# Performance work log

Hardware: AMD Instinct MI355X
Metric: run time of the kernel (lower is better)

The kernel has to match this reference:

```python
import jax, jax.numpy as jnp
import numpy as np

DT = 0.1  # integration step
EPS = 1e-06

def setup_inputs() -> dict:
    key = jax.random.key(0)
    ks = jax.random.split(key, 8)
    B, T, I, H, O = 256, 512, 64, 512, 64
    return {
        'x_seq': jax.random.normal(ks[0], (B, T, I), jnp.float32),
        'W_in0': jax.random.normal(ks[1], (H, I), jnp.float32) * (1.0 / np.sqrt(I)),
        'b_in0': jnp.zeros((H,), jnp.float32),
        'A0':    jax.random.normal(ks[2], (H, H), jnp.float32) * 0.1,
        'tau0':  jnp.ones((H,), jnp.float32),
        'W_in1': jax.random.normal(ks[3], (H, H), jnp.float32) * (1.0 / np.sqrt(H)),
        'b_in1': jnp.zeros((H,), jnp.float32),
        'A1':    jax.random.normal(ks[4], (H, H), jnp.float32) * 0.1,
        'tau1':  jnp.ones((H,), jnp.float32),
        'W_out': jax.random.normal(ks[5], (O, H), jnp.float32) * (1.0 / np.sqrt(H)),
        'b_out': jnp.zeros((O,), jnp.float32),
    }

def _euler(h, drive, A, tau):
    # dh/dt = (1/|tau|+eps) * (-h + tanh(h @ A.T + drive)); Euler step
    inv_tau = 1.0 / (jnp.abs(tau) + EPS)
    dh = inv_tau * (-h + jnp.tanh(h @ A.T + drive))
    return h + DT * dh

def reference(x_seq, W_in0, b_in0, A0, tau0, W_in1, b_in1, A1, tau1, W_out, b_out):
    B, T, _ = x_seq.shape
    H = A0.shape[0]
    # layer-0 input projection is time-independent of hidden state: precompute
    xw = jnp.einsum('bti,hi->bth', x_seq, W_in0) + b_in0  # (B, T, H)

    def step(carry, xw_t):
        h0, h1 = carry
        h0 = _euler(h0, xw_t, A0, tau0)
        h1 = _euler(h1, h0 @ W_in1.T + b_in1, A1, tau1)
        y = h1 @ W_out.T + b_out
        return (h0, h1), y

    h0 = jnp.zeros((B, H), x_seq.dtype)
    h1 = jnp.zeros((B, H), x_seq.dtype)
    _, ys = jax.lax.scan(step, (h0, h1), jnp.swapaxes(xw, 0, 1))  # scan over time
    return jnp.swapaxes(ys, 0, 1)  # (B, T, O)
```

## Files before the change

kernel.cpp:

```cpp
#include <hip/hip_runtime.h>
#include <hip/hip_bf16.h>
#include <stdint.h>

#define B_ 256
#define T_ 512
#define I_ 64
#define H_ 512
#define O_ 64
#define DT_ 0.1f
#define EPS_ 1e-6f
#define SCALE_ 2048.0f
#define INVSCALE_ 4.8828125e-4f

typedef _Float16 f16x8 __attribute__((ext_vector_type(8)));
typedef float    f32x4 __attribute__((ext_vector_type(4)));

__device__ __forceinline__ f32x4 mfma16(f16x8 a, f16x8 b, f32x4 c) {
    return __builtin_amdgcn_mfma_f32_16x16x32_f16(a, b, c, 0, 0, 0);
}
__device__ __forceinline__ float fast_tanh(float x) {
    float e = __expf(2.0f * x);
    return 1.0f - 2.0f / (e + 1.0f);
}
__device__ __forceinline__ bool is_f32_input(const void* tau0) {
    return *(const unsigned int*)tau0 == 0x3F800000u;
}
__device__ __forceinline__ float load_any(const void* p, int i, bool f32) {
    return f32 ? ((const float*)p)[i] : (float)((const __bf16*)p)[i];
}
__device__ __forceinline__ _Float16 f16bits(unsigned short u) {
    union { unsigned short u; _Float16 f; } c; c.u = u; return c.f;
}
__device__ __forceinline__ unsigned short bits16(_Float16 f) {
    union { unsigned short u; _Float16 f; } c; c.f = f; return c.u;
}
__device__ __forceinline__ int bsum8(uint32_t v) {
    return (int)((v & 0xFF) + ((v >> 8) & 0xFF) + ((v >> 16) & 0xFF) + ((v >> 24) & 0xFF));
}
__device__ __forceinline__ int bmax8(uint32_t v) {
    int a = (int)(v & 0xFF), b = (int)((v >> 8) & 0xFF);
    int c = (int)((v >> 16) & 0xFF), d = (int)((v >> 24) & 0xFF);
    int x = a > b ? a : b, y = c > d ? c : d;
    return x > y ? x : y;
}

#define WS_A0H 0u
#define WS_A1H 524288u
#define WS_W1H 1048576u
#define WS_A0L 1572864u
#define WS_A1L 2097152u
#define WS_W1L 2621440u
#define WS_W0H 3145728u
#define WS_W0L 3211264u
#define WS_WOP 3276800u
#define WS_IT0 3407872u
#define WS_IT1 3409920u
#define WS_BI0 3411968u
#define WS_BI1 3414016u
#define WS_BO  3416064u
#define WS_FLGP 3538944u
#define WS_XCD2 3604480u
#define WS_HB0  4194304u
#define WS_HB1  6291456u

__global__ void k_swizzle(const void* __restrict__ src, _Float16* __restrict__ hi,
                          _Float16* __restrict__ lo, int NK, int kshift,
                          const void* __restrict__ tau) {
    bool f32 = is_f32_input(tau);
    int i = blockIdx.x * 256 + threadIdx.x;
    if (i >= NK) return;
    int n = i >> kshift;
    int k = i & ((1 << kshift) - 1);
    float v = load_any(src, i, f32);
    _Float16 h = (_Float16)v;
    _Float16 l = (_Float16)((v - (float)h) * SCALE_);
    int tile = n >> 4, m = n & 15, kk = k >> 5, q = (k >> 3) & 3, j = k & 7;
    int Kst = 1 << (kshift - 5);
    int off = ((tile * Kst + kk) << 9) + (((q << 4) | m) << 3) + j;
    hi[off] = h;
    lo[off] = l;
}

__global__ void k_swzwo(const void* __restrict__ src, _Float16* __restrict__ dst,
                        const void* __restrict__ tau) {
    bool f32 = is_f32_input(tau);
    int i = blockIdx.x * 256 + threadIdx.x;
    if (i >= 65536) return;
    int j = i & 7, l = (i >> 3) & 63, kk = (i >> 9) & 15, cg = i >> 13;
    int m = l & 15, q = l >> 4;
    int k = kk * 32 + q * 8 + j;
    float v = (m < 8) ? load_any(src, (8 * cg + m) * H_ + k, f32) : 0.0f;
    dst[i] = (_Float16)v;
}

__global__ void k_params(const void* t0, const void* t1,
                         const void* b0, const void* b1, const void* bo,
                         float* it0, float* it1, float* b0f, float* b1f, float* bof) {
    bool f32 = is_f32_input(t0);
    int i = threadIdx.x;
    if (i < H_) {
        it0[i] = 1.0f / (fabsf(load_any(t0, i, f32)) + EPS_);
        it1[i] = 1.0f / (fabsf(load_any(t1, i, f32)) + EPS_);
        b0f[i] = load_any(b0, i, f32);
        b1f[i] = load_any(b1, i, f32);
    }
    if (i < O_) bof[i] = load_any(bo, i, f32);
}

__global__ void k_zero(uint32_t* p, int n) {
    int i = blockIdx.x * 256 + threadIdx.x;
    if (i < n) p[i] = 0;
}

__device__ __forceinline__ void waitflag(const uint32_t* p, uint32_t tgt) {
    while (__hip_atomic_load(p, __ATOMIC_RELAXED, __HIP_MEMORY_SCOPE_AGENT) < tgt) { }
    __asm__ __volatile__("" ::: "memory");
}

__global__ __launch_bounds__(256, 1) void liquid_kernel(
    const void* __restrict__ x_seq, const void* __restrict__ tau0probe,
    char* __restrict__ ws, void* __restrict__ out)
{
    __shared__ _Float16 hTh[2][16][520], hTl[2][16][520];
    __shared__ float yscr[4][16][16];
    __shared__ int s_fast;

    const bool f32 = is_f32_input(tau0probe);
    const int tid  = threadIdx.x;
    const int lane = tid & 63;
    const int w    = tid >> 6;
    const int m    = lane & 15;
    const int q    = lane >> 4;
    const int koff = q * 8;
    const int rg   = blockIdx.x;
    const int cg   = blockIdx.y;
    const int chain = blockIdx.z;
    const int r0   = rg * 16;
    const int colg = cg * 64 + w * 16 + m;
    const int tlg  = cg * 4 + w;
    const int c0   = w * 128 + lane;
    const int c1   = c0 + 64;

    uint32_t* ring = (uint32_t*)(ws + WS_HB0);
    uint32_t* hb1  = (uint32_t*)(ws + WS_HB1);
    uint32_t* fpad = (uint32_t*)(ws + WS_FLGP);
    uint32_t* fsf  = fpad +         (size_t)rg * 8 * 32;
    uint32_t* f1f  = fpad + 4096  + (size_t)rg * 8 * 32;
    uint32_t* pg1  = fpad + 12288 + (size_t)rg * 8 * 32;

    {
        uint32_t* xc = (uint32_t*)(ws + WS_XCD2) + (size_t)rg * 32;
        if (tid == 0) {
            int xid = (int)(__builtin_amdgcn_s_getreg((3u << 11) | 20u) & 7u);
            __hip_atomic_fetch_add(xc + (xid >> 2), 1u << (8 * (xid & 3)),
                                   __ATOMIC_RELAXED, __HIP_MEMORY_SCOPE_AGENT);
            uint32_t v0, v1;
            do {
                __builtin_amdgcn_s_sleep(1);
                v0 = __hip_atomic_load(xc,     __ATOMIC_RELAXED, __HIP_MEMORY_SCOPE_AGENT);
                v1 = __hip_atomic_load(xc + 1, __ATOMIC_RELAXED, __HIP_MEMORY_SCOPE_AGENT);
            } while (bsum8(v0) + bsum8(v1) < 16);
            int mx0 = bmax8(v0), mx1 = bmax8(v1);
            s_fast = ((mx0 > mx1 ? mx0 : mx1) == 16) ? 1 : 0;
        }
    }

    const float* bow = (const float*)(ws + WS_BO);
    const float boY  = (m < 8) ? bow[cg * 8 + m] : 0.0f;

    __syncthreads();
    const bool fastp = (s_fast != 0);

    if (chain == 0) {
        const float it0c = ((const float*)(ws + WS_IT0))[colg];
        const float bi0c = ((const float*)(ws + WS_BI0))[colg];
        const size_t fb  = (((size_t)(tlg * 16)) << 9) + (lane << 3);
        const size_t fb0 = (((size_t)(tlg * 2))  << 9) + (lane << 3);
        f16x8 cA0h[16], cA0l[16];
#pragma unroll
        for (int kk = 0; kk < 16; ++kk) {
            cA0h[kk] = *(const f16x8*)((const _Float16*)(ws + WS_A0H) + fb + ((size_t)kk << 9));
            cA0l[kk] = *(const f16x8*)((const _Float16*)(ws + WS_A0L) + fb + ((size_t)kk << 9));
        }
        f16x8 cW0h[2], cW0l[2];
#pragma unroll
        for (int kk = 0; kk < 2; ++kk) {
            cW0h[kk] = *(const f16x8*)((const _Float16*)(ws + WS_W0H) + fb0 + ((size_t)kk << 9));
            cW0l[kk] = *(const f16x8*)((const _Float16*)(ws + WS_W0L) + fb0 + ((size_t)kk << 9));
        }
        const float*  xpf = (const float*) x_seq + (size_t)(r0 + m) * T_ * I_ + koff;
        const __bf16* xpb = (const __bf16*)x_seq + (size_t)(r0 + m) * T_ * I_ + koff;
        float h0m[4] = {0.f, 0.f, 0.f, 0.f};

        f32x4 xf0 = {}, xf1 = {}, xf2 = {}, xf3 = {};
        uint4 xb0 = {}, xb1 = {};
        if (f32) {
            xf0 = *(const f32x4*)(xpf);
            xf1 = *(const f32x4*)(xpf + 4);
            xf2 = *(const f32x4*)(xpf + 32);
            xf3 = *(const f32x4*)(xpf + 36);
        } else {
            xb0 = *(const uint4*)(xpb);
            xb1 = *(const uint4*)(xpb + 32);
        }

        for (int s = 0; s < T_; ++s) {
            const int cur = s & 1;
            const int rs4 = s & 3;
            const int ws4 = (s + 1) & 3;

            waitflag(fsf + (size_t)(2 * w) * 32,     4u * (uint32_t)s);
            waitflag(fsf + (size_t)(2 * w + 1) * 32, 4u * (uint32_t)s);
            uint32_t rv0[16], rv1[16];
            {
                const uint32_t* src = ring + ((size_t)(rs4 * 16 + rg) * 16) * 512;
                if (fastp) {
#pragma unroll
                    for (int k = 0; k < 16; ++k) {
                        rv0[k] = src[(size_t)k * 512 + c0];
                        rv1[k] = src[(size_t)k * 512 + c1];
                    }
                } else {
#pragma unroll
                    for (int k = 0; k < 16; ++k) {
                        rv0[k] = __hip_atomic_load(src + (size_t)k * 512 + c0, __ATOMIC_RELAXED, __HIP_MEMORY_SCOPE_AGENT);
                        rv1[k] = __hip_atomic_load(src + (size_t)k * 512 + c1, __ATOMIC_RELAXED, __HIP_MEMORY_SCOPE_AGENT);
                    }
                }
            }
#pragma unroll
            for (int k = 0; k < 16; ++k) {
                hTh[cur][k][c0] = f16bits((unsigned short)(rv0[k] & 0xFFFFu));
                hTl[cur][k][c0] = f16bits((unsigned short)(rv0[k] >> 16));
                hTh[cur][k][c1] = f16bits((unsigned short)(rv1[k] & 0xFFFFu));
                hTl[cur][k][c1] = f16bits((unsigned short)(rv1[k] >> 16));
            }
            __syncthreads();

            f32x4 a1 = {0.f,0.f,0.f,0.f}, a2 = {0.f,0.f,0.f,0.f}, a3 = {0.f,0.f,0.f,0.f};
#pragma unroll
            for (int kk = 0; kk < 16; ++kk) {
                f16x8 ah = *(const f16x8*)(&hTh[cur][m][kk * 32 + koff]);
                f16x8 al = *(const f16x8*)(&hTl[cur][m][kk * 32 + koff]);
                a1 = mfma16(ah, cA0h[kk], a1);
                a2 = mfma16(ah, cA0l[kk], a2);
                a3 = mfma16(al, cA0h[kk], a3);
            }
            {
                f16x8 xh0, xl0, xh1, xl1;
                if (f32) {
                    float v0[8] = {xf0[0],xf0[1],xf0[2],xf0[3],xf1[0],xf1[1],xf1[2],xf1[3]};
                    float v1[8] = {xf2[0],xf2[1],xf2[2],xf2[3],xf3[0],xf3[1],xf3[2],xf3[3]};
#pragma unroll
                    for (int j = 0; j < 8; ++j) {
                        xh0[j] = (_Float16)v0[j];
                        xl0[j] = (_Float16)((v0[j] - (float)xh0[j]) * SCALE_);
                        xh1[j] = (_Float16)v1[j];
                        xl1[j] = (_Float16)((v1[j] - (float)xh1[j]) * SCALE_);
                    }
                } else {
                    const __bf16* p0 = (const __bf16*)&xb0;
                    const __bf16* p1 = (const __bf16*)&xb1;
#pragma unroll
                    for (int j = 0; j < 8; ++j) {
                        xh0[j] = (_Float16)(float)p0[j]; xl0[j] = (_Float16)0.0f;
                        xh1[j] = (_Float16)(float)p1[j]; xl1[j] = (_Float16)0.0f;
                    }
                }
                a1 = mfma16(xh0, cW0h[0], a1);
                a2 = mfma16(xh0, cW0l[0], a2);
                a3 = mfma16(xl0, cW0h[0], a3);
                a1 = mfma16(xh1, cW0h[1], a1);
                a2 = mfma16(xh1, cW0l[1], a2);
                a3 = mfma16(xl1, cW0h[1], a3);
            }

            if (s >= 3) {
                const uint32_t tgt = 4u * (uint32_t)(s - 3);
                const uint32_t* pp = pg1 + (size_t)(lane & 7) * 32;
                uint32_t v = (lane < 8)
                    ? __hip_atomic_load(pp, __ATOMIC_RELAXED, __HIP_MEMORY_SCOPE_AGENT)
                    : 0xFFFFFFFFu;
                while (__any(v < tgt)) {
                    v = (lane < 8)
                        ? __hip_atomic_load(pp, __ATOMIC_RELAXED, __HIP_MEMORY_SCOPE_AGENT)
                        : 0xFFFFFFFFu;
                }
                __asm__ __volatile__("" ::: "memory");
            }

            uint32_t* dst = ring + ((size_t)(ws4 * 16 + rg) * 16) * 512 + colg;
#pragma unroll
            for (int r = 0; r < 4; ++r) {
                float z = a1[r] + (a2[r] + a3[r]) * INVSCALE_ + bi0c;
                float h = h0m[r];
                h += DT_ * it0c * (fast_tanh(z) - h);
                h0m[r] = h;
                _Float16 hh = (_Float16)h;
                _Float16 hl = (_Float16)((h - (float)hh) * SCALE_);
                uint32_t pk = (uint32_t)bits16(hh) | ((uint32_t)bits16(hl) << 16);
                if (fastp) dst[(size_t)(q * 4 + r) * 512] = pk;
                else __hip_atomic_store(dst + (size_t)(q * 4 + r) * 512, pk,
                                        __ATOMIC_RELAXED, __HIP_MEMORY_SCOPE_AGENT);
            }
            asm volatile("s_waitcnt vmcnt(0)" ::: "memory");
            if (lane == 0)
                __hip_atomic_fetch_add(fsf + (size_t)cg * 32, 1u, __ATOMIC_RELAXED, __HIP_MEMORY_SCOPE_AGENT);

            {
                const int tn = (s + 1 < T_) ? s + 1 : s;
                if (f32) {
                    const float* p = xpf + (size_t)tn * I_;
                    xf0 = *(const f32x4*)(p);
                    xf1 = *(const f32x4*)(p + 4);
                    xf2 = *(const f32x4*)(p + 32);
                    xf3 = *(const f32x4*)(p + 36);
                } else {
                    const __bf16* p = xpb + (size_t)tn * I_;
                    xb0 = *(const uint4*)(p);
                    xb1 = *(const uint4*)(p + 32);
                }
            }
        }
        return;
    }

    {
        const float it1c = ((const float*)(ws + WS_IT1))[colg];
        const float bi1c = ((const float*)(ws + WS_BI1))[colg];
        const size_t fb = (((size_t)(tlg * 16)) << 9) + (lane << 3);
        f16x8 cA1h[16], cA1l[16], cW1h[16], cW1l[16];
#pragma unroll
        for (int kk = 0; kk < 16; ++kk) {
            cA1h[kk] = *(const f16x8*)((const _Float16*)(ws + WS_A1H) + fb + ((size_t)kk << 9));
            cA1l[kk] = *(const f16x8*)((const _Float16*)(ws + WS_A1L) + fb + ((size_t)kk << 9));
            cW1h[kk] = *(const f16x8*)((const _Float16*)(ws + WS_W1H) + fb + ((size_t)kk << 9));
            cW1l[kk] = *(const f16x8*)((const _Float16*)(ws + WS_W1L) + fb + ((size_t)kk << 9));
        }
        const _Float16* pWOP = (const _Float16*)(ws + WS_WOP) + (((size_t)(cg * 16)) << 9) + (lane << 3);
        float h1m[4] = {0.f, 0.f, 0.f, 0.f};

        for (int s = 0; s < T_; ++s) {
            const int cur = s & 1, nxt = (s + 1) & 1;
            const int rs4 = (s + 1) & 3;

            waitflag(f1f + (size_t)(2 * w) * 32,     4u * (uint32_t)s);
            waitflag(f1f + (size_t)(2 * w + 1) * 32, 4u * (uint32_t)s);
            uint32_t rv0[16], rv1[16];
            {
                const uint32_t* src = hb1 + ((size_t)(cur * 16 + rg) * 16) * 512;
                if (fastp) {
#pragma unroll
                    for (int k = 0; k < 16; ++k) {
                        rv0[k] = src[(size_t)k * 512 + c0];
                        rv1[k] = src[(size_t)k * 512 + c1];
                    }
                } else {
#pragma unroll
                    for (int k = 0; k < 16; ++k) {
                        rv0[k] = __hip_atomic_load(src + (size_t)k * 512 + c0, __ATOMIC_RELAXED, __HIP_MEMORY_SCOPE_AGENT);
                        rv1[k] = __hip_atomic_load(src + (size_t)k * 512 + c1, __ATOMIC_RELAXED, __HIP_MEMORY_SCOPE_AGENT);
                    }
                }
            }
            waitflag(fsf + (size_t)(2 * w) * 32,     4u * (uint32_t)(s + 1));
            waitflag(fsf + (size_t)(2 * w + 1) * 32, 4u * (uint32_t)(s + 1));
#pragma unroll
            for (int k = 0; k < 16; ++k) {
                hTh[0][k][c0] = f16bits((unsigned short)(rv0[k] & 0xFFFFu));
                hTl[0][k][c0] = f16bits((unsigned short)(rv0[k] >> 16));
                hTh[0][k][c1] = f16bits((unsigned short)(rv1[k] & 0xFFFFu));
                hTl[0][k][c1] = f16bits((unsigned short)(rv1[k] >> 16));
            }
            __syncthreads();

            {
                const uint32_t* src = ring + ((size_t)(rs4 * 16 + rg) * 16) * 512;
                if (fastp) {
#pragma unroll
                    for (int k = 0; k < 16; ++k) {
                        rv0[k] = src[(size_t)k * 512 + c0];
                        rv1[k] = src[(size_t)k * 512 + c1];
                    }
                } else {
#pragma unroll
                    for (int k = 0; k < 16; ++k) {
                        rv0[k] = __hip_atomic_load(src + (size_t)k * 512 + c0, __ATOMIC_RELAXED, __HIP_MEMORY_SCOPE_AGENT);
                        rv1[k] = __hip_atomic_load(src + (size_t)k * 512 + c1, __ATOMIC_RELAXED, __HIP_MEMORY_SCOPE_AGENT);
                    }
                }
            }

            if (s >= 1) {
                f32x4 y1 = {0.f,0.f,0.f,0.f}, y2 = {0.f,0.f,0.f,0.f};
#pragma unroll
                for (int kk2 = 0; kk2 < 4; ++kk2) {
                    int kk = w * 4 + kk2;
                    f16x8 ah = *(const f16x8*)(&hTh[0][m][kk * 32 + koff]);
                    f16x8 al = *(const f16x8*)(&hTl[0][m][kk * 32 + koff]);
                    f16x8 b  = *(const f16x8*)(pWOP + ((size_t)kk << 9));
                    y1 = mfma16(ah, b, y1);
                    y2 = mfma16(al, b, y2);
                }
#pragma unroll
                for (int r = 0; r < 4; ++r)
                    yscr[w][q * 4 + r][m] = y1[r] + y2[r] * INVSCALE_;
            }

            f32x4 a1 = {0.f,0.f,0.f,0.f}, a2 = {0.f,0.f,0.f,0.f}, a3 = {0.f,0.f,0.f,0.f};
#pragma unroll
            for (int kk = 0; kk < 16; ++kk) {
                f16x8 ah = *(const f16x8*)(&hTh[0][m][kk * 32 + koff]);
                f16x8 al = *(const f16x8*)(&hTl[0][m][kk * 32 + koff]);
                a1 = mfma16(ah, cA1h[kk], a1);
                a2 = mfma16(ah, cA1l[kk], a2);
                a3 = mfma16(al, cA1h[kk], a3);
            }

#pragma unroll
            for (int k = 0; k < 16; ++k) {
                hTh[1][k][c0] = f16bits((unsigned short)(rv0[k] & 0xFFFFu));
                hTl[1][k][c0] = f16bits((unsigned short)(rv0[k] >> 16));
                hTh[1][k][c1] = f16bits((unsigned short)(rv1[k] & 0xFFFFu));
                hTl[1][k][c1] = f16bits((unsigned short)(rv1[k] >> 16));
            }
            if (lane == 0)
                __hip_atomic_fetch_add(pg1 + (size_t)cg * 32, 1u, __ATOMIC_RELAXED, __HIP_MEMORY_SCOPE_AGENT);
            __syncthreads();

#pragma unroll
            for (int kk = 0; kk < 16; ++kk) {
                f16x8 ah = *(const f16x8*)(&hTh[1][m][kk * 32 + koff]);
                f16x8 al = *(const f16x8*)(&hTl[1][m][kk * 32 + koff]);
                a1 = mfma16(ah, cW1h[kk], a1);
                a2 = mfma16(ah, cW1l[kk], a2);
                a3 = mfma16(al, cW1h[kk], a3);
            }

            uint32_t* dst = hb1 + ((size_t)(nxt * 16 + rg) * 16) * 512 + colg;
#pragma unroll
            for (int r = 0; r < 4; ++r) {
                float z = a1[r] + (a2[r] + a3[r]) * INVSCALE_ + bi1c;
                float h = h1m[r];
                h += DT_ * it1c * (fast_tanh(z) - h);
                h1m[r] = h;
                _Float16 hh = (_Float16)h;
                _Float16 hl = (_Float16)((h - (float)hh) * SCALE_);
                uint32_t pk = (uint32_t)bits16(hh) | ((uint32_t)bits16(hl) << 16);
                if (fastp) dst[(size_t)(q * 4 + r) * 512] = pk;
                else __hip_atomic_store(dst + (size_t)(q * 4 + r) * 512, pk,
                                        __ATOMIC_RELAXED, __HIP_MEMORY_SCOPE_AGENT);
            }
            asm volatile("s_waitcnt vmcnt(0)" ::: "memory");
            if (lane == 0)
                __hip_atomic_fetch_add(f1f + (size_t)cg * 32, 1u, __ATOMIC_RELAXED, __HIP_MEMORY_SCOPE_AGENT);

            if (w == 0 && s >= 1 && m < 8) {
#pragma unroll
                for (int r = 0; r < 4; ++r) {
                    float v = yscr[0][q * 4 + r][m] + yscr[1][q * 4 + r][m]
                            + yscr[2][q * 4 + r][m] + yscr[3][q * 4 + r][m] + boY;
                    size_t idx = ((size_t)(r0 + q * 4 + r) * T_ + (s - 1)) * O_ + cg * 8 + m;
                    if (f32) ((float*)out)[idx] = v;
                    else     ((__bf16*)out)[idx] = (__bf16)v;
                }
            }
        }

        waitflag(f1f + (size_t)(2 * w) * 32,     4u * (uint32_t)T_);
        waitflag(f1f + (size_t)(2 * w + 1) * 32, 4u * (uint32_t)T_);
        {
            uint32_t rv0[16], rv1[16];
            const uint32_t* src = hb1 + ((size_t)((T_ & 1) * 16 + rg) * 16) * 512;
            if (fastp) {
#pragma unroll
                for (int k = 0; k < 16; ++k) {
                    rv0[k] = src[(size_t)k * 512 + c0];
                    rv1[k] = src[(size_t)k * 512 + c1];
                }
            } else {
#pragma unroll
                for (int k = 0; k < 16; ++k) {
                    rv0[k] = __hip_atomic_load(src + (size_t)k * 512 + c0, __ATOMIC_RELAXED, __HIP_MEMORY_SCOPE_AGENT);
                    rv1[k] = __hip_atomic_load(src + (size_t)k * 512 + c1, __ATOMIC_RELAXED, __HIP_MEMORY_SCOPE_AGENT);
                }
            }
            __syncthreads();
#pragma unroll
            for (int k = 0; k < 16; ++k) {
                hTh[0][k][c0] = f16bits((unsigned short)(rv0[k] & 0xFFFFu));
                hTl[0][k][c0] = f16bits((unsigned short)(rv0[k] >> 16));
                hTh[0][k][c1] = f16bits((unsigned short)(rv1[k] & 0xFFFFu));
                hTl[0][k][c1] = f16bits((unsigned short)(rv1[k] >> 16));
            }
        }
        __syncthreads();
        {
            f32x4 y1 = {0.f,0.f,0.f,0.f}, y2 = {0.f,0.f,0.f,0.f};
#pragma unroll
            for (int kk2 = 0; kk2 < 4; ++kk2) {
                int kk = w * 4 + kk2;
                f16x8 ah = *(const f16x8*)(&hTh[0][m][kk * 32 + koff]);
                f16x8 al = *(const f16x8*)(&hTl[0][m][kk * 32 + koff]);
                f16x8 b  = *(const f16x8*)(pWOP + ((size_t)kk << 9));
                y1 = mfma16(ah, b, y1);
                y2 = mfma16(al, b, y2);
            }
#pragma unroll
            for (int r = 0; r < 4; ++r)
                yscr[w][q * 4 + r][m] = y1[r] + y2[r] * INVSCALE_;
        }
        __syncthreads();
        if (w == 0 && m < 8) {
#pragma unroll
            for (int r = 0; r < 4; ++r) {
                float v = yscr[0][q * 4 + r][m] + yscr[1][q * 4 + r][m]
                        + yscr[2][q * 4 + r][m] + yscr[3][q * 4 + r][m] + boY;
                size_t idx = ((size_t)(r0 + q * 4 + r) * T_ + (T_ - 1)) * O_ + cg * 8 + m;
                if (f32) ((float*)out)[idx] = v;
                else     ((__bf16*)out)[idx] = (__bf16)v;
            }
        }
    }
}

extern "C" void kernel_launch(void* const* d_in, const int* in_sizes, int n_in,
                              void* d_out, int out_size, void* d_ws, size_t ws_size,
                              hipStream_t stream) {
    const void* x_seq = d_in[0];
    const void* W_in0 = d_in[1];
    const void* b_in0 = d_in[2];
    const void* A0    = d_in[3];
    const void* tau0  = d_in[4];
    const void* W_in1 = d_in[5];
    const void* b_in1 = d_in[6];
    const void* A1    = d_in[7];
    const void* tau1  = d_in[8];
    const void* W_out = d_in[9];
    const void* b_out = d_in[10];

    char* ws = (char*)d_ws;
    const int HH = H_ * H_, HI = H_ * I_;

    k_swizzle<<<(HH + 255) / 256, 256, 0, stream>>>(A0,    (_Float16*)(ws + WS_A0H), (_Float16*)(ws + WS_A0L), HH, 9, tau0);
    k_swizzle<<<(HH + 255) / 256, 256, 0, stream>>>(A1,    (_Float16*)(ws + WS_A1H), (_Float16*)(ws + WS_A1L), HH, 9, tau0);
    k_swizzle<<<(HH + 255) / 256, 256, 0, stream>>>(W_in1, (_Float16*)(ws + WS_W1H), (_Float16*)(ws + WS_W1L), HH, 9, tau0);
    k_swizzle<<<(HI + 255) / 256, 256, 0, stream>>>(W_in0, (_Float16*)(ws + WS_W0H), (_Float16*)(ws + WS_W0L), HI, 6, tau0);
    k_swzwo <<<65536 / 256, 256, 0, stream>>>(W_out, (_Float16*)(ws + WS_WOP), tau0);
    k_params<<<1, 512, 0, stream>>>(tau0, tau1, b_in0, b_in1, b_out,
                                    (float*)(ws + WS_IT0), (float*)(ws + WS_IT1),
                                    (float*)(ws + WS_BI0), (float*)(ws + WS_BI1),
                                    (float*)(ws + WS_BO));
    k_zero<<<(16896 + 255) / 256, 256, 0, stream>>>((uint32_t*)(ws + WS_FLGP), 16896);
    k_zero<<<(786432 + 255) / 256, 256, 0, stream>>>((uint32_t*)(ws + WS_HB0), 786432);

    liquid_kernel<<<dim3(16, 8, 2), dim3(256), 0, stream>>>(x_seq, tau0, ws, d_out);
}
```

Measured before the change: 3.056 ms.

## Halve blocks per row group, widen to 8 waves, and overlap local-slice MFMAs with exchange

Each row group is now split across 4 blocks of 512 threads instead of 8 blocks of 256, so each block owns a quarter of the hidden columns and fewer peers have to synchronise through global flags. Each block writes its own new hidden slice straight into LDS. It starts the recurrent MFMAs on that local k-slice before waiting on peer flags, then loads only the three peer quarters with packed 32-bit LDS stores. The output projection now uses all 16 MFMA columns instead of padding half of them. The cost is more registers per thread, a second barrier each step, and less grid parallelism.

```diff
diff --git a/kernel.cpp b/kernel.cpp
--- a/kernel.cpp
+++ b/kernel.cpp
@@ -28,9 +28,6 @@
 __device__ __forceinline__ float load_any(const void* p, int i, bool f32) {
     return f32 ? ((const float*)p)[i] : (float)((const __bf16*)p)[i];
 }
-__device__ __forceinline__ _Float16 f16bits(unsigned short u) {
-    union { unsigned short u; _Float16 f; } c; c.u = u; return c.f;
-}
 __device__ __forceinline__ unsigned short bits16(_Float16 f) {
     union { unsigned short u; _Float16 f; } c; c.f = f; return c.u;
 }
@@ -42,6 +39,12 @@
     int c = (int)((v >> 16) & 0xFF), d = (int)((v >> 24) & 0xFF);
     int x = a > b ? a : b, y = c > d ? c : d;
     return x > y ? x : y;
+}
+__device__ __forceinline__ uint32_t pack_lo(uint32_t a, uint32_t b) {
+    return (a & 0xFFFFu) | (b << 16);
+}
+__device__ __forceinline__ uint32_t pack_hi(uint32_t a, uint32_t b) {
+    return (a >> 16) | (b & 0xFFFF0000u);
 }
 
 #define WS_A0H 0u
@@ -85,11 +88,11 @@
                         const void* __restrict__ tau) {
     bool f32 = is_f32_input(tau);
     int i = blockIdx.x * 256 + threadIdx.x;
-    if (i >= 65536) return;
-    int j = i & 7, l = (i >> 3) & 63, kk = (i >> 9) & 15, cg = i >> 13;
+    if (i >= 32768) return;
+    int j = i & 7, l = (i >> 3) & 63, kk = (i >> 9) & 15, g = i >> 13;
     int m = l & 15, q = l >> 4;
     int k = kk * 32 + q * 8 + j;
-    float v = (m < 8) ? load_any(src, (8 * cg + m) * H_ + k, f32) : 0.0f;
+    float v = load_any(src, (16 * g + m) * H_ + k, f32);
     dst[i] = (_Float16)v;
 }
 
@@ -116,13 +119,30 @@
     while (__hip_atomic_load(p, __ATOMIC_RELAXED, __HIP_MEMORY_SCOPE_AGENT) < tgt) { }
     __asm__ __volatile__("" ::: "memory");
 }
-
-__global__ __launch_bounds__(256, 1) void liquid_kernel(
+__device__ __forceinline__ uint2 ld2(const uint32_t* p, bool fastp) {
+    if (fastp) return *(const uint2*)p;
+    uint2 r;
+    r.x = __hip_atomic_load(p,     __ATOMIC_RELAXED, __HIP_MEMORY_SCOPE_AGENT);
+    r.y = __hip_atomic_load(p + 1, __ATOMIC_RELAXED, __HIP_MEMORY_SCOPE_AGENT);
+    return r;
+}
+__device__ __forceinline__ uint4 ld4(const uint32_t* p, bool fastp) {
+    if (fastp) return *(const uint4*)p;
+    uint4 r;
+    r.x = __hip_atomic_load(p,     __ATOMIC_RELAXED, __HIP_MEMORY_SCOPE_AGENT);
+    r.y = __hip_atomic_load(p + 1, __ATOMIC_RELAXED, __HIP_MEMORY_SCOPE_AGENT);
+    r.z = __hip_atomic_load(p + 2, __ATOMIC_RELAXED, __HIP_MEMORY_SCOPE_AGENT);
+    r.w = __hip_atomic_load(p + 3, __ATOMIC_RELAXED, __HIP_MEMORY_SCOPE_AGENT);
+    return r;
+}
+
+__global__ __launch_bounds__(512, 1) void liquid_kernel(
     const void* __restrict__ x_seq, const void* __restrict__ tau0probe,
     char* __restrict__ ws, void* __restrict__ out)
 {
     __shared__ _Float16 hTh[2][16][520], hTl[2][16][520];
-    __shared__ float yscr[4][16][16];
+    __shared__ _Float16 hUh[16][520], hUl[16][520];
+    __shared__ float yscr[8][16][16];
     __shared__ int s_fast;
 
     const bool f32 = is_f32_input(tau0probe);
@@ -133,13 +153,13 @@
     const int q    = lane >> 4;
     const int koff = q * 8;
     const int rg   = blockIdx.x;
-    const int cg   = blockIdx.y;
+    const int qt   = blockIdx.y;
     const int chain = blockIdx.z;
     const int r0   = rg * 16;
-    const int colg = cg * 64 + w * 16 + m;
-    const int tlg  = cg * 4 + w;
-    const int c0   = w * 128 + lane;
-    const int c1   = c0 + 64;
+    const int tlg  = qt * 8 + w;
+    const int colg = tlg * 16 + m;
+    const int p0 = (qt + 1) & 3, p1 = (qt + 2) & 3, p2 = (qt + 3) & 3;
+    const int kr1 = w, kr2 = w + 8;
 
     uint32_t* ring = (uint32_t*)(ws + WS_HB0);
     uint32_t* hb1  = (uint32_t*)(ws + WS_HB1);
@@ -147,6 +167,11 @@
     uint32_t* fsf  = fpad +         (size_t)rg * 8 * 32;
     uint32_t* f1f  = fpad + 4096  + (size_t)rg * 8 * 32;
     uint32_t* pg1  = fpad + 12288 + (size_t)rg * 8 * 32;
+
+    for (int i = tid; i < 16 * 520; i += 512) {
+        (&hTh[0][0][0])[i] = (_Float16)0.0f;
+        (&hTl[0][0][0])[i] = (_Float16)0.0f;
+    }
 
     {
         uint32_t* xc = (uint32_t*)(ws + WS_XCD2) + (size_t)rg * 32;
@@ -159,14 +184,11 @@
                 __builtin_amdgcn_s_sleep(1);
                 v0 = __hip_atomic_load(xc,     __ATOMIC_RELAXED, __HIP_MEMORY_SCOPE_AGENT);
                 v1 = __hip_atomic_load(xc + 1, __ATOMIC_RELAXED, __HIP_MEMORY_SCOPE_AGENT);
-            } while (bsum8(v0) + bsum8(v1) < 16);
+            } while (bsum8(v0) + bsum8(v1) < 8);
             int mx0 = bmax8(v0), mx1 = bmax8(v1);
-            s_fast = ((mx0 > mx1 ? mx0 : mx1) == 16) ? 1 : 0;
+            s_fast = ((mx0 > mx1 ? mx0 : mx1) == 8) ? 1 : 0;
         }
     }
-
-    const float* bow = (const float*)(ws + WS_BO);
-    const float boY  = (m < 8) ? bow[cg * 8 + m] : 0.0f;
 
     __syncthreads();
     const bool fastp = (s_fast != 0);
@@ -178,9 +200,10 @@
         const size_t fb0 = (((size_t)(tlg * 2))  << 9) + (lane << 3);
         f16x8 cA0h[16], cA0l[16];
 #pragma unroll
-        for (int kk = 0; kk < 16; ++kk) {
-            cA0h[kk] = *(const f16x8*)((const _Float16*)(ws + WS_A0H) + fb + ((size_t)kk << 9));
-            cA0l[kk] = *(const f16x8*)((const _Float16*)(ws + WS_A0L) + fb + ((size_t)kk << 9));
+        for (int j = 0; j < 16; ++j) {
+            const int kkl = (qt * 4 + j) & 15;
+            cA0h[j] = *(const f16x8*)((const _Float16*)(ws + WS_A0H) + fb + ((size_t)kkl << 9));
+            cA0l[j] = *(const f16x8*)((const _Float16*)(ws + WS_A0L) + fb + ((size_t)kkl << 9));
         }
         f16x8 cW0h[2], cW0l[2];
 #pragma unroll
@@ -205,46 +228,18 @@
         }
 
         for (int s = 0; s < T_; ++s) {
-            const int cur = s & 1;
-            const int rs4 = s & 3;
-            const int ws4 = (s + 1) & 3;
-
-            waitflag(fsf + (size_t)(2 * w) * 32,     4u * (uint32_t)s);
-            waitflag(fsf + (size_t)(2 * w + 1) * 32, 4u * (uint32_t)s);
-            uint32_t rv0[16], rv1[16];
-            {
-                const uint32_t* src = ring + ((size_t)(rs4 * 16 + rg) * 16) * 512;
-                if (fastp) {
-#pragma unroll
-                    for (int k = 0; k < 16; ++k) {
-                        rv0[k] = src[(size_t)k * 512 + c0];
-                        rv1[k] = src[(size_t)k * 512 + c1];
-                    }
-                } else {
-#pragma unroll
-                    for (int k = 0; k < 16; ++k) {
-                        rv0[k] = __hip_atomic_load(src + (size_t)k * 512 + c0, __ATOMIC_RELAXED, __HIP_MEMORY_SCOPE_AGENT);
-                        rv1[k] = __hip_atomic_load(src + (size_t)k * 512 + c1, __ATOMIC_RELAXED, __HIP_MEMORY_SCOPE_AGENT);
-                    }
-                }
-            }
-#pragma unroll
-            for (int k = 0; k < 16; ++k) {
-                hTh[cur][k][c0] = f16bits((unsigned short)(rv0[k] & 0xFFFFu));
-                hTl[cur][k][c0] = f16bits((unsigned short)(rv0[k] >> 16));
-                hTh[cur][k][c1] = f16bits((unsigned short)(rv1[k] & 0xFFFFu));
-                hTl[cur][k][c1] = f16bits((unsigned short)(rv1[k] >> 16));
-            }
-            __syncthreads();
+            const int cur = s & 1, nxt = (s + 1) & 1;
+            const int rs4 = s & 3, ws4 = (s + 1) & 3;
 
             f32x4 a1 = {0.f,0.f,0.f,0.f}, a2 = {0.f,0.f,0.f,0.f}, a3 = {0.f,0.f,0.f,0.f};
 #pragma unroll
-            for (int kk = 0; kk < 16; ++kk) {
-                f16x8 ah = *(const f16x8*)(&hTh[cur][m][kk * 32 + koff]);
-                f16x8 al = *(const f16x8*)(&hTl[cur][m][kk * 32 + koff]);
-                a1 = mfma16(ah, cA0h[kk], a1);
-                a2 = mfma16(ah, cA0l[kk], a2);
-                a3 = mfma16(al, cA0h[kk], a3);
+            for (int j = 0; j < 4; ++j) {
+                const int kkl = qt * 4 + j;
+                f16x8 ah = *(const f16x8*)(&hTh[cur][m][kkl * 32 + koff]);
+                f16x8 al = *(const f16x8*)(&hTl[cur][m][kkl * 32 + koff]);
+                a1 = mfma16(ah, cA0h[j], a1);
+                a2 = mfma16(ah, cA0l[j], a2);
+                a3 = mfma16(al, cA0h[j], a3);
             }
             {
                 f16x8 xh0, xl0, xh1, xl1;
@@ -259,12 +254,12 @@
                         xl1[j] = (_Float16)((v1[j] - (float)xh1[j]) * SCALE_);
                     }
                 } else {
-                    const __bf16* p0 = (const __bf16*)&xb0;
-                    const __bf16* p1 = (const __bf16*)&xb1;
+                    const __bf16* pp0 = (const __bf16*)&xb0;
+                    const __bf16* pp1 = (const __bf16*)&xb1;
 #pragma unroll
                     for (int j = 0; j < 8; ++j) {
-                        xh0[j] = (_Float16)(float)p0[j]; xl0[j] = (_Float16)0.0f;
-                        xh1[j] = (_Float16)(float)p1[j]; xl1[j] = (_Float16)0.0f;
+                        xh0[j] = (_Float16)(float)pp0[j]; xl0[j] = (_Float16)0.0f;
+                        xh1[j] = (_Float16)(float)pp1[j]; xl1[j] = (_Float16)0.0f;
                     }
                 }
                 a1 = mfma16(xh0, cW0h[0], a1);
@@ -275,14 +270,54 @@
                 a3 = mfma16(xl1, cW0h[1], a3);
             }
 
+            {
+                waitflag(fsf + (size_t)p0 * 32, 8u * (uint32_t)s);
+                waitflag(fsf + (size_t)p1 * 32, 8u * (uint32_t)s);
+                waitflag(fsf + (size_t)p2 * 32, 8u * (uint32_t)s);
+                const uint32_t* gsrc = ring + ((size_t)(rs4 * 16 + rg) * 16) * 512;
+                uint2 gA0 = ld2(gsrc + (size_t)kr1 * 512 + p0 * 128 + lane * 2, fastp);
+                uint2 gA1 = ld2(gsrc + (size_t)kr1 * 512 + p1 * 128 + lane * 2, fastp);
+                uint2 gA2 = ld2(gsrc + (size_t)kr1 * 512 + p2 * 128 + lane * 2, fastp);
+                uint2 gB0 = ld2(gsrc + (size_t)kr2 * 512 + p0 * 128 + lane * 2, fastp);
+                uint2 gB1 = ld2(gsrc + (size_t)kr2 * 512 + p1 * 128 + lane * 2, fastp);
+                uint2 gB2 = ld2(gsrc + (size_t)kr2 * 512 + p2 * 128 + lane * 2, fastp);
+                asm volatile("s_waitcnt vmcnt(0)" ::: "memory");
+                const int c0 = p0 * 128 + lane * 2;
+                const int c1 = p1 * 128 + lane * 2;
+                const int c2 = p2 * 128 + lane * 2;
+                *(uint32_t*)&hTh[cur][kr1][c0] = pack_lo(gA0.x, gA0.y);
+                *(uint32_t*)&hTl[cur][kr1][c0] = pack_hi(gA0.x, gA0.y);
+                *(uint32_t*)&hTh[cur][kr1][c1] = pack_lo(gA1.x, gA1.y);
+                *(uint32_t*)&hTl[cur][kr1][c1] = pack_hi(gA1.x, gA1.y);
+                *(uint32_t*)&hTh[cur][kr1][c2] = pack_lo(gA2.x, gA2.y);
+                *(uint32_t*)&hTl[cur][kr1][c2] = pack_hi(gA2.x, gA2.y);
+                *(uint32_t*)&hTh[cur][kr2][c0] = pack_lo(gB0.x, gB0.y);
+                *(uint32_t*)&hTl[cur][kr2][c0] = pack_hi(gB0.x, gB0.y);
+                *(uint32_t*)&hTh[cur][kr2][c1] = pack_lo(gB1.x, gB1.y);
+                *(uint32_t*)&hTl[cur][kr2][c1] = pack_hi(gB1.x, gB1.y);
+                *(uint32_t*)&hTh[cur][kr2][c2] = pack_lo(gB2.x, gB2.y);
+                *(uint32_t*)&hTl[cur][kr2][c2] = pack_hi(gB2.x, gB2.y);
+            }
+            __syncthreads();
+
+#pragma unroll
+            for (int j = 4; j < 16; ++j) {
+                const int kkl = (qt * 4 + j) & 15;
+                f16x8 ah = *(const f16x8*)(&hTh[cur][m][kkl * 32 + koff]);
+                f16x8 al = *(const f16x8*)(&hTl[cur][m][kkl * 32 + koff]);
+                a1 = mfma16(ah, cA0h[j], a1);
+                a2 = mfma16(ah, cA0l[j], a2);
+                a3 = mfma16(al, cA0h[j], a3);
+            }
+
             if (s >= 3) {
-                const uint32_t tgt = 4u * (uint32_t)(s - 3);
-                const uint32_t* pp = pg1 + (size_t)(lane & 7) * 32;
-                uint32_t v = (lane < 8)
+                const uint32_t tgt = 8u * (uint32_t)(s - 3);
+                const uint32_t* pp = pg1 + (size_t)(lane & 3) * 32;
+                uint32_t v = (lane < 4)
                     ? __hip_atomic_load(pp, __ATOMIC_RELAXED, __HIP_MEMORY_SCOPE_AGENT)
                     : 0xFFFFFFFFu;
                 while (__any(v < tgt)) {
-                    v = (lane < 8)
+                    v = (lane < 4)
                         ? __hip_atomic_load(pp, __ATOMIC_RELAXED, __HIP_MEMORY_SCOPE_AGENT)
                         : 0xFFFFFFFFu;
                 }
@@ -302,10 +337,14 @@
                 if (fastp) dst[(size_t)(q * 4 + r) * 512] = pk;
                 else __hip_atomic_store(dst + (size_t)(q * 4 + r) * 512, pk,
                                         __ATOMIC_RELAXED, __HIP_MEMORY_SCOPE_AGENT);
+                hTh[nxt][q * 4 + r][colg] = hh;
+                hTl[nxt][q * 4 + r][colg] = hl;
             }
             asm volatile("s_waitcnt vmcnt(0)" ::: "memory");
             if (lane == 0)
-                __hip_atomic_fetch_add(fsf + (size_t)cg * 32, 1u, __ATOMIC_RELAXED, __HIP_MEMORY_SCOPE_AGENT);
+                __hip_atomic_fetch_add(fsf + (size_t)qt * 32, 1u, __ATOMIC_RELAXED,
+                                       __HIP_MEMORY_SCOPE_AGENT);
+            __syncthreads();
 
             {
                 const int tn = (s + 1 < T_) ? s + 1 : s;
@@ -328,76 +367,106 @@
     {
         const float it1c = ((const float*)(ws + WS_IT1))[colg];
         const float bi1c = ((const float*)(ws + WS_BI1))[colg];
+        const float* bow = (const float*)(ws + WS_BO);
+        const float boY  = bow[qt * 16 + m];
         const size_t fb = (((size_t)(tlg * 16)) << 9) + (lane << 3);
         f16x8 cA1h[16], cA1l[16], cW1h[16], cW1l[16];
 #pragma unroll
-        for (int kk = 0; kk < 16; ++kk) {
-            cA1h[kk] = *(const f16x8*)((const _Float16*)(ws + WS_A1H) + fb + ((size_t)kk << 9));
-            cA1l[kk] = *(const f16x8*)((const _Float16*)(ws + WS_A1L) + fb + ((size_t)kk << 9));
-            cW1h[kk] = *(const f16x8*)((const _Float16*)(ws + WS_W1H) + fb + ((size_t)kk << 9));
-            cW1l[kk] = *(const f16x8*)((const _Float16*)(ws + WS_W1L) + fb + ((size_t)kk << 9));
-        }
-        const _Float16* pWOP = (const _Float16*)(ws + WS_WOP) + (((size_t)(cg * 16)) << 9) + (lane << 3);
+        for (int j = 0; j < 16; ++j) {
+            const int kkl = (qt * 4 + j) & 15;
+            cA1h[j] = *(const f16x8*)((const _Float16*)(ws + WS_A1H) + fb + ((size_t)kkl << 9));
+            cA1l[j] = *(const f16x8*)((const _Float16*)(ws + WS_A1L) + fb + ((size_t)kkl << 9));
+            cW1h[j] = *(const f16x8*)((const _Float16*)(ws + WS_W1H) + fb + ((size_t)j << 9));
+            cW1l[j] = *(const f16x8*)((const _Float16*)(ws + WS_W1L) + fb + ((size_t)j << 9));
+        }
+        const _Float16* pWOP = (const _Float16*)(ws + WS_WOP)
+                             + (((size_t)(qt * 16)) << 9) + (lane << 3);
         float h1m[4] = {0.f, 0.f, 0.f, 0.f};
 
         for (int s = 0; s < T_; ++s) {
             const int cur = s & 1, nxt = (s + 1) & 1;
             const int rs4 = (s + 1) & 3;
 
-            waitflag(f1f + (size_t)(2 * w) * 32,     4u * (uint32_t)s);
-            waitflag(f1f + (size_t)(2 * w + 1) * 32, 4u * (uint32_t)s);
-            uint32_t rv0[16], rv1[16];
+            f32x4 a1 = {0.f,0.f,0.f,0.f}, a2 = {0.f,0.f,0.f,0.f}, a3 = {0.f,0.f,0.f,0.f};
+#pragma unroll
+            for (int j = 0; j < 4; ++j) {
+                const int kkl = qt * 4 + j;
+                f16x8 ah = *(const f16x8*)(&hTh[cur][m][kkl * 32 + koff]);
+                f16x8 al = *(const f16x8*)(&hTl[cur][m][kkl * 32 + koff]);
+                a1 = mfma16(ah, cA1h[j], a1);
+                a2 = mfma16(ah, cA1l[j], a2);
+                a3 = mfma16(al, cA1h[j], a3);
+            }
+
             {
-                const uint32_t* src = hb1 + ((size_t)(cur * 16 + rg) * 16) * 512;
-                if (fastp) {
-#pragma unroll
-                    for (int k = 0; k < 16; ++k) {
-                        rv0[k] = src[(size_t)k * 512 + c0];
-                        rv1[k] = src[(size_t)k * 512 + c1];
-                    }
-                } else {
-#pragma unroll
-                    for (int k = 0; k < 16; ++k) {
-                        rv0[k] = __hip_atomic_load(src + (size_t)k * 512 + c0, __ATOMIC_RELAXED, __HIP_MEMORY_SCOPE_AGENT);
-                        rv1[k] = __hip_atomic_load(src + (size_t)k * 512 + c1, __ATOMIC_RELAXED, __HIP_MEMORY_SCOPE_AGENT);
-                    }
-                }
-            }
-            waitflag(fsf + (size_t)(2 * w) * 32,     4u * (uint32_t)(s + 1));
-            waitflag(fsf + (size_t)(2 * w + 1) * 32, 4u * (uint32_t)(s + 1));
-#pragma unroll
-            for (int k = 0; k < 16; ++k) {
-                hTh[0][k][c0] = f16bits((unsigned short)(rv0[k] & 0xFFFFu));
-                hTl[0][k][c0] = f16bits((unsigned short)(rv0[k] >> 16));
-                hTh[0][k][c1] = f16bits((unsigned short)(rv1[k] & 0xFFFFu));
-                hTl[0][k][c1] = f16bits((unsigned short)(rv1[k] >> 16));
-            }
+                waitflag(f1f + (size_t)p0 * 32, 8u * (uint32_t)s);
+                waitflag(f1f + (size_t)p1 * 32, 8u * (uint32_t)s);
+                waitflag(f1f + (size_t)p2 * 32, 8u * (uint32_t)s);
+                const uint32_t* hsrc = hb1 + ((size_t)(cur * 16 + rg) * 16) * 512;
+                uint2 gA0 = ld2(hsrc + (size_t)kr1 * 512 + p0 * 128 + lane * 2, fastp);
+                uint2 gA1 = ld2(hsrc + (size_t)kr1 * 512 + p1 * 128 + lane * 2, fastp);
+                uint2 gA2 = ld2(hsrc + (size_t)kr1 * 512 + p2 * 128 + lane * 2, fastp);
+                uint2 gB0 = ld2(hsrc + (size_t)kr2 * 512 + p0 * 128 + lane * 2, fastp);
+                uint2 gB1 = ld2(hsrc + (size_t)kr2 * 512 + p1 * 128 + lane * 2, fastp);
+                uint2 gB2 = ld2(hsrc + (size_t)kr2 * 512 + p2 * 128 + lane * 2, fastp);
+
+                waitflag(fsf + 0 * 32,  8u * (uint32_t)(s + 1));
+                waitflag(fsf + 1 * 32,  8u * (uint32_t)(s + 1));
+                waitflag(fsf + 2 * 32,  8u * (uint32_t)(s + 1));
+                waitflag(fsf + 3 * 32,  8u * (uint32_t)(s + 1));
+                const uint32_t* rsrc = ring + ((size_t)(rs4 * 16 + rg) * 16) * 512;
+                uint4 uA0 = ld4(rsrc + (size_t)kr1 * 512 + lane * 8,     fastp);
+                uint4 uA1 = ld4(rsrc + (size_t)kr1 * 512 + lane * 8 + 4, fastp);
+                uint4 uB0 = ld4(rsrc + (size_t)kr2 * 512 + lane * 8,     fastp);
+                uint4 uB1 = ld4(rsrc + (size_t)kr2 * 512 + lane * 8 + 4, fastp);
+                asm volatile("s_waitcnt vmcnt(0)" ::: "memory");
+
+                const int c0 = p0 * 128 + lane * 2;
+                const int c1 = p1 * 128 + lane * 2;
+                const int c2 = p2 * 128 + lane * 2;
+                *(uint32_t*)&hTh[cur][kr1][c0] = pack_lo(gA0.x, gA0.y);
+                *(uint32_t*)&hTl[cur][kr1][c0] = pack_hi(gA0.x, gA0.y);
+                *(uint32_t*)&hTh[cur][kr1][c1] = pack_lo(gA1.x, gA1.y);
+                *(uint32_t*)&hTl[cur][kr1][c1] = pack_hi(gA1.x, gA1.y);
+                *(uint32_t*)&hTh[cur][kr1][c2] = pack_lo(gA2.x, gA2.y);
+                *(uint32_t*)&hTl[cur][kr1][c2] = pack_hi(gA2.x, gA2.y);
+                *(uint32_t*)&hTh[cur][kr2][c0] = pack_lo(gB0.x, gB0.y);
+                *(uint32_t*)&hTl[cur][kr2][c0] = pack_hi(gB0.x, gB0.y);
+                *(uint32_t*)&hTh[cur][kr2][c1] = pack_lo(gB1.x, gB1.y);
+                *(uint32_t*)&hTl[cur][kr2][c1] = pack_hi(gB1.x, gB1.y);
+                *(uint32_t*)&hTh[cur][kr2][c2] = pack_lo(gB2.x, gB2.y);
+                *(uint32_t*)&hTl[cur][kr2][c2] = pack_hi(gB2.x, gB2.y);
+
+                const int cu = lane * 8;
+                *(uint32_t*)&hUh[kr1][cu]     = pack_lo(uA0.x, uA0.y);
+                *(uint32_t*)&hUl[kr1][cu]     = pack_hi(uA0.x, uA0.y);
+                *(uint32_t*)&hUh[kr1][cu + 2] = pack_lo(uA0.z, uA0.w);
+                *(uint32_t*)&hUl[kr1][cu + 2] = pack_hi(uA0.z, uA0.w);
+                *(uint32_t*)&hUh[kr1][cu + 4] = pack_lo(uA1.x, uA1.y);
+                *(uint32_t*)&hUl[kr1][cu + 4] = pack_hi(uA1.x, uA1.y);
+                *(uint32_t*)&hUh[kr1][cu + 6] = pack_lo(uA1.z, uA1.w);
+                *(uint32_t*)&hUl[kr1][cu + 6] = pack_hi(uA1.z, uA1.w);
+                *(uint32_t*)&hUh[kr2][cu]     = pack_lo(uB0.x, uB0.y);
+                *(uint32_t*)&hUl[kr2][cu]     = pack_hi(uB0.x, uB0.y);
+                *(uint32_t*)&hUh[kr2][cu + 2] = pack_lo(uB0.z, uB0.w);
+                *(uint32_t*)&hUl[kr2][cu + 2] = pack_hi(uB0.z, uB0.w);
+                *(uint32_t*)&hUh[kr2][cu + 4] = pack_lo(uB1.x, uB1.y);
+                *(uint32_t*)&hUl[kr2][cu + 4] = pack_hi(uB1.x, uB1.y);
+                *(uint32_t*)&hUh[kr2][cu + 6] = pack_lo(uB1.z, uB1.w);
+                *(uint32_t*)&hUl[kr2][cu + 6] = pack_hi(uB1.z, uB1.w);
+            }
+            if (lane == 0)
+                __hip_atomic_fetch_add(pg1 + (size_t)qt * 32, 1u, __ATOMIC_RELAXED,
+                                       __HIP_MEMORY_SCOPE_AGENT);
             __syncthreads();
-
-            {
-                const uint32_t* src = ring + ((size_t)(rs4 * 16 + rg) * 16) * 512;
-                if (fastp) {
-#pragma unroll
-                    for (int k = 0; k < 16; ++k) {
-                        rv0[k] = src[(size_t)k * 512 + c0];
-                        rv1[k] = src[(size_t)k * 512 + c1];
-                    }
-                } else {
-#pragma unroll
-                    for (int k = 0; k < 16; ++k) {
-                        rv0[k] = __hip_atomic_load(src + (size_t)k * 512 + c0, __ATOMIC_RELAXED, __HIP_MEMORY_SCOPE_AGENT);
-                        rv1[k] = __hip_atomic_load(src + (size_t)k * 512 + c1, __ATOMIC_RELAXED, __HIP_MEMORY_SCOPE_AGENT);
-                    }
-                }
-            }
 
             if (s >= 1) {
                 f32x4 y1 = {0.f,0.f,0.f,0.f}, y2 = {0.f,0.f,0.f,0.f};
 #pragma unroll
-                for (int kk2 = 0; kk2 < 4; ++kk2) {
-                    int kk = w * 4 + kk2;
-                    f16x8 ah = *(const f16x8*)(&hTh[0][m][kk * 32 + koff]);
-                    f16x8 al = *(const f16x8*)(&hTl[0][m][kk * 32 + koff]);
+                for (int t = 0; t < 2; ++t) {
+                    const int kk = 2 * w + t;
+                    f16x8 ah = *(const f16x8*)(&hTh[cur][m][kk * 32 + koff]);
+                    f16x8 al = *(const f16x8*)(&hTl[cur][m][kk * 32 + koff]);
                     f16x8 b  = *(const f16x8*)(pWOP + ((size_t)kk << 9));
                     y1 = mfma16(ah, b, y1);
                     y2 = mfma16(al, b, y2);
@@ -406,35 +475,22 @@
                 for (int r = 0; r < 4; ++r)
                     yscr[w][q * 4 + r][m] = y1[r] + y2[r] * INVSCALE_;
             }
-
-            f32x4 a1 = {0.f,0.f,0.f,0.f}, a2 = {0.f,0.f,0.f,0.f}, a3 = {0.f,0.f,0.f,0.f};
-#pragma unroll
-            for (int kk = 0; kk < 16; ++kk) {
-                f16x8 ah = *(const f16x8*)(&hTh[0][m][kk * 32 + koff]);
-                f16x8 al = *(const f16x8*)(&hTl[0][m][kk * 32 + koff]);
-                a1 = mfma16(ah, cA1h[kk], a1);
-                a2 = mfma16(ah, cA1l[kk], a2);
-                a3 = mfma16(al, cA1h[kk], a3);
-            }
-
-#pragma unroll
-            for (int k = 0; k < 16; ++k) {
-                hTh[1][k][c0] = f16bits((unsigned short)(rv0[k] & 0xFFFFu));
-                hTl[1][k][c0] = f16bits((unsigned short)(rv0[k] >> 16));
-                hTh[1][k][c1] = f16bits((unsigned short)(rv1[k] & 0xFFFFu));
-                hTl[1][k][c1] = f16bits((unsigned short)(rv1[k] >> 16));
-            }
-            if (lane == 0)
-                __hip_atomic_fetch_add(pg1 + (size_t)cg * 32, 1u, __ATOMIC_RELAXED, __HIP_MEMORY_SCOPE_AGENT);
-            __syncthreads();
-
-#pragma unroll
-            for (int kk = 0; kk < 16; ++kk) {
-                f16x8 ah = *(const f16x8*)(&hTh[1][m][kk * 32 + koff]);
-                f16x8 al = *(const f16x8*)(&hTl[1][m][kk * 32 + koff]);
-                a1 = mfma16(ah, cW1h[kk], a1);
-                a2 = mfma16(ah, cW1l[kk], a2);
-                a3 = mfma16(al, cW1h[kk], a3);
+#pragma unroll
+            for (int j = 4; j < 16; ++j) {
+                const int kkl = (qt * 4 + j) & 15;
+                f16x8 ah = *(const f16x8*)(&hTh[cur][m][kkl * 32 + koff]);
+                f16x8 al = *(const f16x8*)(&hTl[cur][m][kkl * 32 + koff]);
+                a1 = mfma16(ah, cA1h[j], a1);
+                a2 = mfma16(ah, cA1l[j], a2);
+                a3 = mfma16(al, cA1h[j], a3);
+            }
+#pragma unroll
+            for (int j = 0; j < 16; ++j) {
+                f16x8 bh = *(const f16x8*)(&hUh[m][j * 32 + koff]);
+                f16x8 bl = *(const f16x8*)(&hUl[m][j * 32 + koff]);
+                a1 = mfma16(bh, cW1h[j], a1);
+                a2 = mfma16(bh, cW1l[j], a2);
+                a3 = mfma16(bl, cW1h[j], a3);
             }
 
             uint32_t* dst = hb1 + ((size_t)(nxt * 16 + rg) * 16) * 512 + colg;
@@ -450,75 +506,85 @@
                 if (fastp) dst[(size_t)(q * 4 + r) * 512] = pk;
                 else __hip_atomic_store(dst + (size_t)(q * 4 + r) * 512, pk,
                                         __ATOMIC_RELAXED, __HIP_MEMORY_SCOPE_AGENT);
+                hTh[nxt][q * 4 + r][colg] = hh;
+                hTl[nxt][q * 4 + r][colg] = hl;
             }
             asm volatile("s_waitcnt vmcnt(0)" ::: "memory");
             if (lane == 0)
-                __hip_atomic_fetch_add(f1f + (size_t)cg * 32, 1u, __ATOMIC_RELAXED, __HIP_MEMORY_SCOPE_AGENT);
-
-            if (w == 0 && s >= 1 && m < 8) {
+                __hip_atomic_fetch_add(f1f + (size_t)qt * 32, 1u, __ATOMIC_RELAXED,
+                                       __HIP_MEMORY_SCOPE_AGENT);
+            __syncthreads();
+
+            if (w == 0 && s >= 1) {
 #pragma unroll
                 for (int r = 0; r < 4; ++r) {
                     float v = yscr[0][q * 4 + r][m] + yscr[1][q * 4 + r][m]
-                            + yscr[2][q * 4 + r][m] + yscr[3][q * 4 + r][m] + boY;
-                    size_t idx = ((size_t)(r0 + q * 4 + r) * T_ + (s - 1)) * O_ + cg * 8 + m;
+                            + yscr[2][q * 4 + r][m] + yscr[3][q * 4 + r][m]
+                            + yscr[4][q * 4 + r][m] + yscr[5][q * 4 + r][m]
+                            + yscr[6][q * 4 + r][m] + yscr[7][q * 4 + r][m] + boY;
+                    size_t idx = ((size_t)(r0 + q * 4 + r) * T_ + (s - 1)) * O_ + qt * 16 + m;
                     if (f32) ((float*)out)[idx] = v;
                     else     ((__bf16*)out)[idx] = (__bf16)v;
                 }
             }
         }
 
-        waitflag(f1f + (size_t)(2 * w) * 32,     4u * (uint32_t)T_);
-        waitflag(f1f + (size_t)(2 * w + 1) * 32, 4u * (uint32_t)T_);
         {
-            uint32_t rv0[16], rv1[16];
-            const uint32_t* src = hb1 + ((size_t)((T_ & 1) * 16 + rg) * 16) * 512;
-            if (fastp) {
-#pragma unroll
-                for (int k = 0; k < 16; ++k) {
-                    rv0[k] = src[(size_t)k * 512 + c0];
-                    rv1[k] = src[(size_t)k * 512 + c1];
+            const int cur = T_ & 1;
+            waitflag(f1f + (size_t)p0 * 32, 8u * (uint32_t)T_);
+            waitflag(f1f + (size_t)p1 * 32, 8u * (uint32_t)T_);
+            waitflag(f1f + (size_t)p2 * 32, 8u * (uint32_t)T_);
+            const uint32_t* hsrc = hb1 + ((size_t)(cur * 16 + rg) * 16) * 512;
+            uint2 gA0 = ld2(hsrc + (size_t)kr1 * 512 + p0 * 128 + lane * 2, fastp);
+            uint2 gA1 = ld2(hsrc + (size_t)kr1 * 512 + p1 * 128 + lane * 2, fastp);
+            uint2 gA2 = ld2(hsrc + (size_t)kr1 * 512 + p2 * 128 + lane * 2, fastp);
+            uint2 gB0 = ld2(hsrc + (size_t)kr2 * 512 + p0 * 128 + lane * 2, fastp);
+            uint2 gB1 = ld2(hsrc + (size_t)kr2 * 512 + p1 * 128 + lane * 2, fastp);
+            uint2 gB2 = ld2(hsrc + (size_t)kr2 * 512 + p2 * 128 + lane * 2, fastp);
+            asm volatile("s_waitcnt vmcnt(0)" ::: "memory");
+            const int c0 = p0 * 128 + lane * 2;
+            const int c1 = p1 * 128 + lane * 2;
+            const int c2 = p2 * 128 + lane * 2;
+            *(uint32_t*)&hTh[cur][kr1][c0] = pack_lo(gA0.x, gA0.y);
+            *(uint32_t*)&hTl[cur][kr1][c0] = pack_hi(gA0.x, gA0.y);
+            *(uint32_t*)&hTh[cur][kr1][c1] = pack_lo(gA1.x, gA1.y);
+            *(uint32_t*)&hTl[cur][kr1][c1] = pack_hi(gA1.x, gA1.y);
+            *(uint32_t*)&hTh[cur][kr1][c2] = pack_lo(gA2.x, gA2.y);
+            *(uint32_t*)&hTl[cur][kr1][c2] = pack_hi(gA2.x, gA2.y);
+            *(uint32_t*)&hTh[cur][kr2][c0] = pack_lo(gB0.x, gB0.y);
+            *(uint32_t*)&hTl[cur][kr2][c0] = pack_hi(gB0.x, gB0.y);
+            *(uint32_t*)&hTh[cur][kr2][c1] = pack_lo(gB1.x, gB1.y);
+            *(uint32_t*)&hTl[cur][kr2][c1] = pack_hi(gB1.x, gB1.y);
+            *(uint32_t*)&hTh[cur][kr2][c2] = pack_lo(gB2.x, gB2.y);
+            *(uint32_t*)&hTl[cur][kr2][c2] = pack_hi(gB2.x, gB2.y);
+            __syncthreads();
+            {
+                f32x4 y1 = {0.f,0.f,0.f,0.f}, y2 = {0.f,0.f,0.f,0.f};
+#pragma unroll
+                for (int t = 0; t < 2; ++t) {
+                    const int kk = 2 * w + t;
+                    f16x8 ah = *(const f16x8*)(&hTh[cur][m][kk * 32 + koff]);
+                    f16x8 al = *(const f16x8*)(&hTl[cur][m][kk * 32 + koff]);
+                    f16x8 b  = *(const f16x8*)(pWOP + ((size_t)kk << 9));
+                    y1 = mfma16(ah, b, y1);
+                    y2 = mfma16(al, b, y2);
                 }
-            } else {
-#pragma unroll
-                for (int k = 0; k < 16; ++k) {
-                    rv0[k] = __hip_atomic_load(src + (size_t)k * 512 + c0, __ATOMIC_RELAXED, __HIP_MEMORY_SCOPE_AGENT);
-                    rv1[k] = __hip_atomic_load(src + (size_t)k * 512 + c1, __ATOMIC_RELAXED, __HIP_MEMORY_SCOPE_AGENT);
+#pragma unroll
+                for (int r = 0; r < 4; ++r)
+                    yscr[w][q * 4 + r][m] = y1[r] + y2[r] * INVSCALE_;
+            }
+            __syncthreads();
+            if (w == 0) {
+#pragma unroll
+                for (int r = 0; r < 4; ++r) {
+                    float v = yscr[0][q * 4 + r][m] + yscr[1][q * 4 + r][m]
+                            + yscr[2][q * 4 + r][m] + yscr[3][q * 4 + r][m]
+                            + yscr[4][q * 4 + r][m] + yscr[5][q * 4 + r][m]
+                            + yscr[6][q * 4 + r][m] + yscr[7][q * 4 + r][m] + boY;
+                    size_t idx = ((size_t)(r0 + q * 4 + r) * T_ + (T_ - 1)) * O_ + qt * 16 + m;
+                    if (f32) ((float*)out)[idx] = v;
+                    else     ((__bf16*)out)[idx] = (__bf16)v;
                 }
-            }
-            __syncthreads();
-#pragma unroll
-            for (int k = 0; k < 16; ++k) {
-                hTh[0][k][c0] = f16bits((unsigned short)(rv0[k] & 0xFFFFu));
-                hTl[0][k][c0] = f16bits((unsigned short)(rv0[k] >> 16));
-                hTh[0][k][c1] = f16bits((unsigned short)(rv1[k] & 0xFFFFu));
-                hTl[0][k][c1] = f16bits((unsigned short)(rv1[k] >> 16));
-            }
-        }
-        __syncthreads();
-        {
-            f32x4 y1 = {0.f,0.f,0.f,0.f}, y2 = {0.f,0.f,0.f,0.f};
-#pragma unroll
-            for (int kk2 = 0; kk2 < 4; ++kk2) {
-                int kk = w * 4 + kk2;
-                f16x8 ah = *(const f16x8*)(&hTh[0][m][kk * 32 + koff]);
-                f16x8 al = *(const f16x8*)(&hTl[0][m][kk * 32 + koff]);
-                f16x8 b  = *(const f16x8*)(pWOP + ((size_t)kk << 9));
-                y1 = mfma16(ah, b, y1);
-                y2 = mfma16(al, b, y2);
-            }
-#pragma unroll
-            for (int r = 0; r < 4; ++r)
-                yscr[w][q * 4 + r][m] = y1[r] + y2[r] * INVSCALE_;
-        }
-        __syncthreads();
-        if (w == 0 && m < 8) {
-#pragma unroll
-            for (int r = 0; r < 4; ++r) {
-                float v = yscr[0][q * 4 + r][m] + yscr[1][q * 4 + r][m]
-                        + yscr[2][q * 4 + r][m] + yscr[3][q * 4 + r][m] + boY;
-                size_t idx = ((size_t)(r0 + q * 4 + r) * T_ + (T_ - 1)) * O_ + cg * 8 + m;
-                if (f32) ((float*)out)[idx] = v;
-                else     ((__bf16*)out)[idx] = (__bf16)v;
             }
         }
     }
@@ -546,7 +612,7 @@
     k_swizzle<<<(HH + 255) / 256, 256, 0, stream>>>(A1,    (_Float16*)(ws + WS_A1H), (_Float16*)(ws + WS_A1L), HH, 9, tau0);
     k_swizzle<<<(HH + 255) / 256, 256, 0, stream>>>(W_in1, (_Float16*)(ws + WS_W1H), (_Float16*)(ws + WS_W1L), HH, 9, tau0);
     k_swizzle<<<(HI + 255) / 256, 256, 0, stream>>>(W_in0, (_Float16*)(ws + WS_W0H), (_Float16*)(ws + WS_W0L), HI, 6, tau0);
-    k_swzwo <<<65536 / 256, 256, 0, stream>>>(W_out, (_Float16*)(ws + WS_WOP), tau0);
+    k_swzwo <<<32768 / 256, 256, 0, stream>>>(W_out, (_Float16*)(ws + WS_WOP), tau0);
     k_params<<<1, 512, 0, stream>>>(tau0, tau1, b_in0, b_in1, b_out,
                                     (float*)(ws + WS_IT0), (float*)(ws + WS_IT1),
                                     (float*)(ws + WS_BI0), (float*)(ws + WS_BI1),
@@ -554,5 +620,5 @@
     k_zero<<<(16896 + 255) / 256, 256, 0, stream>>>((uint32_t*)(ws + WS_FLGP), 16896);
     k_zero<<<(786432 + 255) / 256, 256, 0, stream>>>((uint32_t*)(ws + WS_HB0), 786432);
 
-    liquid_kernel<<<dim3(16, 8, 2), dim3(256), 0, stream>>>(x_seq, tau0, ws, d_out);
-}
+    liquid_kernel<<<dim3(16, 4, 2), dim3(512), 0, stream>>>(x_seq, tau0, ws, d_out);
+}
```

Result: slower. 6.810 ms (+122.8%).
